# Kernel optimization log

Measured on AMD Instinct MI355X. Metric: run time of the kernel, lower is better.

The kernel has to match this reference:

```python
import jax, jax.numpy as jnp
import numpy as np

B, C, H, W = 8, 256, 64, 64
IC = C // 2  # inter_channel


def setup_inputs() -> dict:
    key = jax.random.key(0)
    k0, k1, k2, k3, k4 = jax.random.split(key, 5)
    s = 0.05
    return {
        "x": jax.random.normal(k0, (B, C, H, W), dtype=jnp.float32),
        "w_theta": jax.random.normal(k1, (IC, C), dtype=jnp.float32) * s,
        "w_phi": jax.random.normal(k2, (IC, C), dtype=jnp.float32) * s,
        "w_g": jax.random.normal(k3, (IC, C), dtype=jnp.float32) * s,
        "w_mask": jax.random.normal(k4, (C, IC), dtype=jnp.float32) * s,
    }


def reference(x, w_theta, w_phi, w_g, w_mask):
    b, c, h, w = x.shape
    ic = c // 2
    # 1x1 convs (bias=False) == channel-mixing einsums -> (b, ic, h, w)
    theta = jnp.einsum("oc,bchw->bohw", w_theta, x)
    phi = jnp.einsum("oc,bchw->bohw", w_phi, x)
    g = jnp.einsum("oc,bchw->bohw", w_g, x)
    # Faithful to original: .view(b, c, -1) on a (b, ic, h, w) tensor
    # => sequence length N = h*w/2, feature dim = c (full channels).
    n = ic * h * w // c  # = h*w/2
    x_theta = theta.reshape(b, c, n).transpose(0, 2, 1)  # (b, n, c)
    x_phi = phi.reshape(b, c, n)                          # (b, c, n)
    x_g = g.reshape(b, c, n).transpose(0, 2, 1)           # (b, n, c)
    attn = jnp.matmul(x_theta, x_phi)                     # (b, n, n)
    # Original uses nn.Softmax(dim=1): normalize over ROWS, not last axis.
    attn = jax.nn.softmax(attn, axis=1)
    out = jnp.matmul(attn, x_g)                           # (b, n, c)
    out = out.transpose(0, 2, 1).reshape(b, ic, h, w)     # (b, ic, h, w)
    mask = jnp.einsum("oc,bchw->bohw", w_mask, out)       # (b, c, h, w)
    return mask + x
```

## Files before the change

kernel.cpp:

```cpp
#include <hip/hip_runtime.h>

typedef __attribute__((ext_vector_type(8))) __bf16 bf16x8;
typedef __attribute__((ext_vector_type(4))) float f32x4;

#define LOG2E 1.4426950408889634f

#define OTA_OFF  0ul
#define TT_OFF   16777216ul
#define PT_OFF   25165824ul
#define G_OFF    33554432ul
#define W3_OFF   41943040ul
#define WM_OFF   42139648ul
#define ID_OFF   42205184ul
#define PART_OFF 42270720ul
#define WS_NEED  44367872ul

__device__ __forceinline__ void gload16(const __bf16* g, __bf16* l){
  __builtin_amdgcn_global_load_lds((const __attribute__((address_space(1))) void*)g,
                                   (__attribute__((address_space(3))) void*)l, 16, 0, 0);
}

__global__ __launch_bounds__(256) void k_weights(const float* wt, const float* wp,
                                                 const float* wg, const float* wm,
                                                 __bf16* W3, __bf16* Wm){
  int idx = blockIdx.x*256 + threadIdx.x;
  if (idx < 98304){
    float v = (idx < 32768) ? wt[idx] : (idx < 65536) ? wp[idx - 32768] : wg[idx - 65536];
    W3[idx] = (__bf16)v;
  } else if (idx < 131072){
    Wm[idx - 98304] = (__bf16)wm[idx - 98304];
  }
}

__global__ __launch_bounds__(512, 2) void k_conv3x(const float* x, const __bf16* W3,
                                                   __bf16* Tt, __bf16* Pt, __bf16* G){
  __shared__ __bf16 As[128*256];
  __shared__ __bf16 Bs[2][64*256];
  __shared__ float  tf[64*65];
  int bid = blockIdx.x;
  int b = bid & 7, m = bid >> 3, p0 = m*128;
  int tid = threadIdx.x, lane = tid & 63, w = tid >> 6;
  int lr = lane & 15, kq = lane >> 4;
  int pw = w & 1, ow4 = w >> 1;
  const float* xb = x + (size_t)b*256*4096 + p0;
  int sRow2 = lane >> 5, sSlot = lane & 31;
  #pragma unroll
  for (int u = 0; u < 4; ++u){
    int row = u*16 + w*2 + sRow2;
    gload16(W3 + (size_t)row*256 + ((sSlot ^ (row & 7))*8), &Bs[0][(u*16 + w*2)*256]);
  }
  #pragma unroll
  for (int st = 0; st < 8; ++st){
    int ct = st >> 1, pt = st & 1;
    int c0 = ct*64, ps = pt*64;
    #pragma unroll
    for (int u = 0; u < 2; ++u){
      int idx = u*512 + tid;
      int row = idx >> 4, col4 = (idx & 15)*4;
      f32x4 v = *(const f32x4*)(xb + (size_t)(c0 + row)*4096 + ps + col4);
      #pragma unroll
      for (int e = 0; e < 4; ++e) tf[row*65 + col4 + e] = v[e];
    }
    __syncthreads();
    {
      int pl = tid & 63, slot8 = tid >> 6;
      __bf16 pk[8];
      #pragma unroll
      for (int e = 0; e < 8; ++e) pk[e] = (__bf16)tf[(slot8*8 + e)*65 + pl];
      int row = ps + pl, slotIdx = ct*8 + slot8;
      *(uint4*)&As[row*256 + ((slotIdx ^ (row & 7))*8)] = *(const uint4*)pk;
    }
    __syncthreads();
  }
  bf16x8 aReg[4][8];
  #pragma unroll
  for (int fm = 0; fm < 4; ++fm){
    int ar = pw*64 + fm*16 + lr;
    #pragma unroll
    for (int sl = 0; sl < 8; ++sl){
      int slotA = (sl >> 1)*8 + (sl & 1)*4 + kq;
      aReg[fm][sl] = *(const bf16x8*)&As[ar*256 + ((slotA ^ (ar & 7))*8)];
    }
  }
  for (int ot = 0; ot < 6; ++ot){
    if (ot < 5){
      int buf = (ot + 1) & 1;
      #pragma unroll
      for (int u = 0; u < 4; ++u){
        int row = u*16 + w*2 + sRow2;
        gload16(W3 + (size_t)((ot+1)*64 + row)*256 + ((sSlot ^ (row & 7))*8),
                &Bs[buf][(u*16 + w*2)*256]);
      }
    }
    const __bf16* Bc = &Bs[ot & 1][0];
    f32x4 acc[4] = {};
    #pragma unroll
    for (int kc = 0; kc < 4; ++kc)
      #pragma unroll
      for (int ks = 0; ks < 2; ++ks){
        int slotB = kc*8 + ks*4 + kq;
        int br = ow4*16 + lr;
        bf16x8 bf = *(const bf16x8*)&Bc[br*256 + ((slotB ^ (br & 7))*8)];
        #pragma unroll
        for (int fm = 0; fm < 4; ++fm)
          acc[fm] = __builtin_amdgcn_mfma_f32_16x16x32_bf16(aReg[fm][kc*2+ks], bf, acc[fm], 0, 0, 0);
      }
    #pragma unroll
    for (int fm = 0; fm < 4; ++fm)
      #pragma unroll
      for (int r = 0; r < 4; ++r){
        int p = p0 + pw*64 + fm*16 + kq*4 + r;
        int o = ot*64 + ow4*16 + lr;
        __bf16 v = (__bf16)acc[fm][r];
        int i = p & 2047, ph = p >> 11;
        if (o < 128)      Tt[((size_t)b*2048 + i)*256 + 2*o + ph] = v;
        else if (o < 256) Pt[((size_t)b*2048 + i)*256 + 2*(o-128) + ph] = v;
        else              G [((size_t)b*256 + 2*(o-256) + ph)*2048 + i] = v;
      }
    __syncthreads();
  }
}

__global__ __launch_bounds__(512, 2) void k_sexp(const __bf16* Tt, const __bf16* Pt,
                                                 __bf16* S, float* PART, int js0){
  __shared__ __bf16 As[64*256];
  __shared__ __bf16 Bs[8][3][2048];
  int bid = blockIdx.x;
  int b = bid & 7, m = bid >> 3, m0 = m*64;
  int tid = threadIdx.x, lane = tid & 63, w = tid >> 6;
  int lr = lane & 15, kq = lane >> 4;
  const __bf16* Ab = Tt + ((size_t)b*2048 + m0)*256;
  const __bf16* Pb = Pt + ((size_t)b*2048 + js0)*256;
  __bf16* Sb = S + ((size_t)b*2048 + m0)*1024;
  {
    int aRow = lane >> 5, aSlot = lane & 31;
    #pragma unroll
    for (int u = 0; u < 4; ++u){
      int row = w*8 + u*2 + aRow;
      gload16(Ab + (size_t)row*256 + ((aSlot ^ (row & 7))*8), &As[w*2048 + u*512]);
    }
  }
  int bRow = lane >> 3, bSlot = lane & 7;
  #pragma unroll
  for (int s0 = 0; s0 < 2; ++s0){
    int j0 = (w + (s0 >> 2)*8)*32, kc = s0 & 3;
    #pragma unroll
    for (int u = 0; u < 4; ++u){
      int row = j0 + u*8 + bRow;
      gload16(Pb + (size_t)row*256 + kc*64 + ((bSlot ^ (row & 7))*8), &Bs[w][s0][u*512]);
    }
  }
  __syncthreads();
  bf16x8 aReg[4][8];
  #pragma unroll
  for (int fm = 0; fm < 4; ++fm){
    int ar = fm*16 + lr;
    #pragma unroll
    for (int sl = 0; sl < 8; ++sl){
      int slotA = (sl >> 1)*8 + (sl & 1)*4 + kq;
      aReg[fm][sl] = *(const bf16x8*)&As[ar*256 + ((slotA ^ (ar & 7))*8)];
    }
  }
  for (int q = 0; q < 4; ++q){
    int j0 = (w + q*8)*32;
    f32x4 acc[4][2] = {};
    #pragma unroll
    for (int kc = 0; kc < 4; ++kc){
      int s = q*4 + kc;
      if (s == 15) asm volatile("s_waitcnt vmcnt(0)" ::: "memory");
      else         asm volatile("s_waitcnt vmcnt(4)" ::: "memory");
      if (s + 2 < 16){
        int s2 = s + 2, q2 = s2 >> 2, kc2 = s2 & 3, rb = s2 % 3;
        int j02 = (w + q2*8)*32;
        #pragma unroll
        for (int u = 0; u < 4; ++u){
          int row = j02 + u*8 + bRow;
          gload16(Pb + (size_t)row*256 + kc2*64 + ((bSlot ^ (row & 7))*8), &Bs[w][rb][u*512]);
        }
      }
      const __bf16* Bc = &Bs[w][s % 3][0];
      #pragma unroll
      for (int ks = 0; ks < 2; ++ks){
        int slotB = ks*4 + kq;
        bf16x8 bf[2];
        #pragma unroll
        for (int fn = 0; fn < 2; ++fn){
          int br = fn*16 + lr;
          bf[fn] = *(const bf16x8*)&Bc[br*64 + ((slotB ^ (br & 7))*8)];
        }
        #pragma unroll
        for (int fm = 0; fm < 4; ++fm)
          #pragma unroll
          for (int fn = 0; fn < 2; ++fn)
            acc[fm][fn] = __builtin_amdgcn_mfma_f32_16x16x32_bf16(aReg[fm][kc*2+ks], bf[fn], acc[fm][fn], 0, 0, 0);
      }
    }
    #pragma unroll
    for (int fn = 0; fn < 2; ++fn){
      float v = 0.f;
      #pragma unroll
      for (int fm = 0; fm < 4; ++fm){
        #pragma unroll
        for (int r = 0; r < 4; ++r){
          float e = exp2f(acc[fm][fn][r] * LOG2E);
          v += e;
          Sb[(size_t)(fm*16 + kq*4 + r)*1024 + j0 + fn*16 + lr] = (__bf16)e;
        }
      }
      v += __shfl_xor(v, 16);
      v += __shfl_xor(v, 32);
      if (kq == 0)
        PART[((size_t)b*32 + m)*1024 + j0 + fn*16 + lr] = v;
    }
  }
}

__global__ __launch_bounds__(256) void k_invd(const float* PART, float* invD, int js0){
  int bid = blockIdx.x;
  int b = bid & 7, seg = bid >> 3;
  int jl = seg*256 + threadIdx.x;
  float s = 0.f;
  #pragma unroll
  for (int it = 0; it < 32; ++it) s += PART[((size_t)b*32 + it)*1024 + jl];
  invD[(size_t)b*2048 + js0 + jl] = 1.0f / s;
}

__global__ __launch_bounds__(256) void k_gscale(__bf16* G, const float* invD, int js0){
  int bid = blockIdx.x;
  int b = bid >> 8, c = bid & 255;
  int jl = threadIdx.x * 4;
  __bf16* gp = G + ((size_t)b*256 + c)*2048 + js0 + jl;
  const float* dp = invD + (size_t)b*2048 + js0 + jl;
  f32x4 d = *(const f32x4*)dp;
  __bf16 gv[4];
  *(uint2*)gv = *(const uint2*)gp;
  #pragma unroll
  for (int e = 0; e < 4; ++e) gv[e] = (__bf16)((float)gv[e] * d[e]);
  *(uint2*)gp = *(const uint2*)gv;
}

__global__ __launch_bounds__(256) void k_pv(const __bf16* S, const __bf16* G,
                                            float* OTacc, int js0, int first){
  __shared__ __bf16 sA[3][128*64];
  __shared__ __bf16 sB[3][64*64];
  int bid = blockIdx.x;
  int b = bid & 7, r2 = bid >> 3;
  int n = r2 & 3, m = r2 >> 2;
  int m0 = m*128, n0 = n*64;
  int tid = threadIdx.x, lane = tid & 63, w = tid >> 6;
  int lr = lane & 15, kq = lane >> 4;
  int wm = w >> 1, wn = w & 1;
  const __bf16* Ab = S + ((size_t)b*2048 + m0)*1024;
  const __bf16* Bb = G + ((size_t)b*256 + n0)*2048 + js0;
  int bRow = lane >> 3, bSlot = lane & 7;
  f32x4 acc[4][2] = {};
  #pragma unroll
  for (int t0 = 0; t0 < 2; ++t0){
    #pragma unroll
    for (int u = 0; u < 4; ++u){
      int row = u*32 + w*8 + bRow;
      gload16(Ab + (size_t)row*1024 + t0*64 + ((bSlot ^ (row & 7))*8),
              &sA[t0][u*2048 + w*512]);
    }
    #pragma unroll
    for (int u = 0; u < 2; ++u){
      int row = u*32 + w*8 + bRow;
      gload16(Bb + (size_t)row*2048 + t0*64 + ((bSlot ^ (row & 7))*8),
              &sB[t0][u*2048 + w*512]);
    }
  }
  for (int t = 0; t < 16; ++t){
    if (t == 15) asm volatile("s_waitcnt vmcnt(0)" ::: "memory");
    else         asm volatile("s_waitcnt vmcnt(6)" ::: "memory");
    __builtin_amdgcn_s_barrier();
    if (t + 2 < 16){
      int t2 = t + 2, bf2 = t2 % 3, k0 = t2*64;
      #pragma unroll
      for (int u = 0; u < 4; ++u){
        int row = u*32 + w*8 + bRow;
        gload16(Ab + (size_t)row*1024 + k0 + ((bSlot ^ (row & 7))*8),
                &sA[bf2][u*2048 + w*512]);
      }
      #pragma unroll
      for (int u = 0; u < 2; ++u){
        int row = u*32 + w*8 + bRow;
        gload16(Bb + (size_t)row*2048 + k0 + ((bSlot ^ (row & 7))*8),
                &sB[bf2][u*2048 + w*512]);
      }
    }
    const __bf16* Ac = &sA[t % 3][0];
    const __bf16* Bc = &sB[t % 3][0];
    #pragma unroll
    for (int ks = 0; ks < 2; ++ks){
      int slot = ks*4 + kq;
      bf16x8 af[4], bf[2];
      #pragma unroll
      for (int fm = 0; fm < 4; ++fm){
        int ar = wm*64 + fm*16 + lr;
        af[fm] = *(const bf16x8*)&Ac[ar*64 + ((slot ^ (ar & 7))*8)];
      }
      #pragma unroll
      for (int fn = 0; fn < 2; ++fn){
        int br = wn*32 + fn*16 + lr;
        bf[fn] = *(const bf16x8*)&Bc[br*64 + ((slot ^ (br & 7))*8)];
      }
      #pragma unroll
      for (int fm = 0; fm < 4; ++fm)
        #pragma unroll
        for (int fn = 0; fn < 2; ++fn)
          acc[fm][fn] = __builtin_amdgcn_mfma_f32_16x16x32_bf16(af[fm], bf[fn], acc[fm][fn], 0, 0, 0);
    }
  }
  float* Ob = OTacc + (size_t)b*4096*128;
  if (first){
    #pragma unroll
    for (int fm = 0; fm < 4; ++fm)
      #pragma unroll
      for (int fn = 0; fn < 2; ++fn)
        #pragma unroll
        for (int r = 0; r < 4; ++r){
          int i = m0 + wm*64 + fm*16 + kq*4 + r;
          int c = n0 + wn*32 + fn*16 + lr;
          Ob[(size_t)(((c & 1) << 11) + i)*128 + (c >> 1)] = acc[fm][fn][r];
        }
  } else {
    #pragma unroll
    for (int fm = 0; fm < 4; ++fm)
      #pragma unroll
      for (int fn = 0; fn < 2; ++fn)
        #pragma unroll
        for (int r = 0; r < 4; ++r){
          int i = m0 + wm*64 + fm*16 + kq*4 + r;
          int c = n0 + wn*32 + fn*16 + lr;
          size_t idx = (size_t)(((c & 1) << 11) + i)*128 + (c >> 1);
          Ob[idx] += acc[fm][fn][r];
        }
  }
}

__global__ __launch_bounds__(256) void k_mask(const float* OTacc, const __bf16* Wm,
                                              const float* x, float* out){
  __shared__ __bf16 As[128*72];
  __shared__ __bf16 Bs[64*72];
  int b = blockIdx.z, p0 = blockIdx.x*128, o0 = blockIdx.y*64;
  int tid = threadIdx.x, lane = tid & 63, wave = tid >> 6;
  int wm = wave >> 1, wn = wave & 1;
  f32x4 acc[4][2] = {};
  const float* Ab = OTacc + ((size_t)b*4096 + p0)*128;
  const __bf16* Bb = Wm + (size_t)o0*128;
  for (int kc = 0; kc < 2; ++kc){
    int k0 = kc*64;
    #pragma unroll
    for (int it = 0; it < 8; ++it){
      int idx = it*256 + tid;
      int row = idx >> 4, c4 = (idx & 15)*4;
      f32x4 vv = *(const f32x4*)(Ab + (size_t)row*128 + k0 + c4);
      __bf16 tmp[4];
      #pragma unroll
      for (int e = 0; e < 4; ++e) tmp[e] = (__bf16)vv[e];
      *(uint2*)&As[row*72 + c4] = *(const uint2*)tmp;
    }
    #pragma unroll
    for (int itc = 0; itc < 2; ++itc){
      int s = tid + itc*256, row = s >> 3, sk = s & 7;
      *(uint4*)&Bs[row*72 + sk*8] = *(const uint4*)(Bb + (size_t)row*128 + k0 + sk*8);
    }
    __syncthreads();
    #pragma unroll
    for (int ks = 0; ks < 2; ++ks){
      int koff = ks*32 + (lane>>4)*8;
      bf16x8 af[4], bfr[2];
      #pragma unroll
      for (int fm = 0; fm < 4; ++fm)
        af[fm] = *(const bf16x8*)&As[(wm*64 + fm*16 + (lane&15))*72 + koff];
      #pragma unroll
      for (int fn = 0; fn < 2; ++fn)
        bfr[fn] = *(const bf16x8*)&Bs[(wn*32 + fn*16 + (lane&15))*72 + koff];
      #pragma unroll
      for (int fm = 0; fm < 4; ++fm)
        #pragma unroll
        for (int fn = 0; fn < 2; ++fn)
          acc[fm][fn] = __builtin_amdgcn_mfma_f32_16x16x32_bf16(af[fm], bfr[fn], acc[fm][fn], 0, 0, 0);
    }
    __syncthreads();
  }
  #pragma unroll
  for (int fm = 0; fm < 4; ++fm)
    #pragma unroll
    for (int fn = 0; fn < 2; ++fn){
      int pb = p0 + wm*64 + fm*16 + (lane>>4)*4;
      int o = o0 + wn*32 + fn*16 + (lane&15);
      size_t idx = ((size_t)b*256 + o)*4096 + pb;
      f32x4 xv = *(const f32x4*)(x + idx);
      f32x4 ov = acc[fm][fn] + xv;
      *(f32x4*)(out + idx) = ov;
    }
}

extern "C" void kernel_launch(void* const* d_in, const int* in_sizes, int n_in,
                              void* d_out, int out_size, void* d_ws, size_t ws_size,
                              hipStream_t stream){
  if (ws_size < WS_NEED) return;
  const float* x  = (const float*)d_in[0];
  const float* wt = (const float*)d_in[1];
  const float* wp = (const float*)d_in[2];
  const float* wg = (const float*)d_in[3];
  const float* wm = (const float*)d_in[4];
  char* ws = (char*)d_ws;
  float* OTacc = (float*)(ws + OTA_OFF);
  __bf16* Tt   = (__bf16*)(ws + TT_OFF);
  __bf16* Pt   = (__bf16*)(ws + PT_OFF);
  __bf16* G    = (__bf16*)(ws + G_OFF);
  __bf16* W3   = (__bf16*)(ws + W3_OFF);
  __bf16* Wm   = (__bf16*)(ws + WM_OFF);
  float* invD  = (float*)(ws + ID_OFF);
  float* PART  = (float*)(ws + PART_OFF);
  __bf16* S    = (__bf16*)d_out;
  float* out   = (float*)d_out;

  k_weights<<<512, 256, 0, stream>>>(wt, wp, wg, wm, W3, Wm);
  k_conv3x<<<256, 512, 0, stream>>>(x, W3, Tt, Pt, G);
  for (int s = 0; s < 2; ++s){
    int js0 = s * 1024;
    k_sexp<<<256, 512, 0, stream>>>(Tt, Pt, S, PART, js0);
    k_invd<<<32, 256, 0, stream>>>(PART, invD, js0);
    k_gscale<<<2048, 256, 0, stream>>>(G, invD, js0);
    k_pv<<<512, 256, 0, stream>>>(S, G, OTacc, js0, s == 0 ? 1 : 0);
  }
  k_mask<<<dim3(32, 4, 8), 256, 0, stream>>>(OTacc, Wm, x, out);
}
```

Measured before the change: 134.7 us.

## Load A fragments directly to registers and deepen B prefetch to four stages

```diff
diff --git a/kernel.cpp b/kernel.cpp
--- a/kernel.cpp
+++ b/kernel.cpp
@@ -123,62 +123,51 @@
 
 __global__ __launch_bounds__(512, 2) void k_sexp(const __bf16* Tt, const __bf16* Pt,
                                                  __bf16* S, float* PART, int js0){
-  __shared__ __bf16 As[64*256];
-  __shared__ __bf16 Bs[8][3][2048];
+  __shared__ __bf16 Bs[8][4][2048];
   int bid = blockIdx.x;
   int b = bid & 7, m = bid >> 3, m0 = m*64;
   int tid = threadIdx.x, lane = tid & 63, w = tid >> 6;
   int lr = lane & 15, kq = lane >> 4;
-  const __bf16* Ab = Tt + ((size_t)b*2048 + m0)*256;
+  const __bf16* Tb = Tt + ((size_t)b*2048 + m0)*256;
   const __bf16* Pb = Pt + ((size_t)b*2048 + js0)*256;
   __bf16* Sb = S + ((size_t)b*2048 + m0)*1024;
-  {
-    int aRow = lane >> 5, aSlot = lane & 31;
-    #pragma unroll
-    for (int u = 0; u < 4; ++u){
-      int row = w*8 + u*2 + aRow;
-      gload16(Ab + (size_t)row*256 + ((aSlot ^ (row & 7))*8), &As[w*2048 + u*512]);
-    }
-  }
+  bf16x8 aReg[4][8];
+  #pragma unroll
+  for (int fm = 0; fm < 4; ++fm)
+    #pragma unroll
+    for (int sl = 0; sl < 8; ++sl)
+      aReg[fm][sl] = *(const bf16x8*)(Tb + (size_t)(fm*16 + lr)*256
+                                      + (sl >> 1)*64 + (sl & 1)*32 + kq*8);
   int bRow = lane >> 3, bSlot = lane & 7;
   #pragma unroll
-  for (int s0 = 0; s0 < 2; ++s0){
-    int j0 = (w + (s0 >> 2)*8)*32, kc = s0 & 3;
+  for (int s0 = 0; s0 < 3; ++s0){
+    int j0 = w*32, kc = s0;
     #pragma unroll
     for (int u = 0; u < 4; ++u){
       int row = j0 + u*8 + bRow;
       gload16(Pb + (size_t)row*256 + kc*64 + ((bSlot ^ (row & 7))*8), &Bs[w][s0][u*512]);
     }
   }
-  __syncthreads();
-  bf16x8 aReg[4][8];
-  #pragma unroll
-  for (int fm = 0; fm < 4; ++fm){
-    int ar = fm*16 + lr;
-    #pragma unroll
-    for (int sl = 0; sl < 8; ++sl){
-      int slotA = (sl >> 1)*8 + (sl & 1)*4 + kq;
-      aReg[fm][sl] = *(const bf16x8*)&As[ar*256 + ((slotA ^ (ar & 7))*8)];
-    }
-  }
   for (int q = 0; q < 4; ++q){
     int j0 = (w + q*8)*32;
     f32x4 acc[4][2] = {};
     #pragma unroll
     for (int kc = 0; kc < 4; ++kc){
       int s = q*4 + kc;
-      if (s == 15) asm volatile("s_waitcnt vmcnt(0)" ::: "memory");
-      else         asm volatile("s_waitcnt vmcnt(4)" ::: "memory");
-      if (s + 2 < 16){
-        int s2 = s + 2, q2 = s2 >> 2, kc2 = s2 & 3, rb = s2 % 3;
+      if (s < 14)       asm volatile("s_waitcnt vmcnt(8)" ::: "memory");
+      else if (s == 14) asm volatile("s_waitcnt vmcnt(4)" ::: "memory");
+      else              asm volatile("s_waitcnt vmcnt(0)" ::: "memory");
+      if (s + 3 < 16){
+        int s2 = s + 3, q2 = s2 >> 2, kc2 = s2 & 3;
         int j02 = (w + q2*8)*32;
         #pragma unroll
         for (int u = 0; u < 4; ++u){
           int row = j02 + u*8 + bRow;
-          gload16(Pb + (size_t)row*256 + kc2*64 + ((bSlot ^ (row & 7))*8), &Bs[w][rb][u*512]);
+          gload16(Pb + (size_t)row*256 + kc2*64 + ((bSlot ^ (row & 7))*8),
+                  &Bs[w][s2 & 3][u*512]);
         }
       }
-      const __bf16* Bc = &Bs[w][s % 3][0];
+      const __bf16* Bc = &Bs[w][s & 3][0];
       #pragma unroll
       for (int ks = 0; ks < 2; ++ks){
         int slotB = ks*4 + kq;
```

After: 142.5 us. 5.8% more time.

## Halve k_sexp row tile and double-buffer P to raise occupancy

Applied to the files above, without the earlier changes.

```diff
diff --git a/kernel.cpp b/kernel.cpp
--- a/kernel.cpp
+++ b/kernel.cpp
@@ -121,12 +121,12 @@
   }
 }
 
-__global__ __launch_bounds__(512, 2) void k_sexp(const __bf16* Tt, const __bf16* Pt,
+__global__ __launch_bounds__(512, 4) void k_sexp(const __bf16* Tt, const __bf16* Pt,
                                                  __bf16* S, float* PART, int js0){
-  __shared__ __bf16 As[64*256];
-  __shared__ __bf16 Bs[8][3][2048];
+  __shared__ __bf16 As[32*256];
+  __shared__ __bf16 Bs[8][2][2048];
   int bid = blockIdx.x;
-  int b = bid & 7, m = bid >> 3, m0 = m*64;
+  int b = bid & 7, m = bid >> 3, m0 = m*32;
   int tid = threadIdx.x, lane = tid & 63, w = tid >> 6;
   int lr = lane & 15, kq = lane >> 4;
   const __bf16* Ab = Tt + ((size_t)b*2048 + m0)*256;
@@ -135,71 +135,68 @@
   {
     int aRow = lane >> 5, aSlot = lane & 31;
     #pragma unroll
-    for (int u = 0; u < 4; ++u){
-      int row = w*8 + u*2 + aRow;
-      gload16(Ab + (size_t)row*256 + ((aSlot ^ (row & 7))*8), &As[w*2048 + u*512]);
+    for (int u = 0; u < 2; ++u){
+      int row = w*4 + u*2 + aRow;
+      gload16(Ab + (size_t)row*256 + ((aSlot ^ (row & 7))*8), &As[w*1024 + u*512]);
     }
   }
   int bRow = lane >> 3, bSlot = lane & 7;
-  #pragma unroll
-  for (int s0 = 0; s0 < 2; ++s0){
-    int j0 = (w + (s0 >> 2)*8)*32, kc = s0 & 3;
+  {
+    int j0 = w*32;
     #pragma unroll
     for (int u = 0; u < 4; ++u){
       int row = j0 + u*8 + bRow;
-      gload16(Pb + (size_t)row*256 + kc*64 + ((bSlot ^ (row & 7))*8), &Bs[w][s0][u*512]);
+      gload16(Pb + (size_t)row*256 + ((bSlot ^ (row & 7))*8), &Bs[w][0][u*512]);
     }
   }
   __syncthreads();
-  bf16x8 aReg[4][8];
-  #pragma unroll
-  for (int fm = 0; fm < 4; ++fm){
-    int ar = fm*16 + lr;
-    #pragma unroll
-    for (int sl = 0; sl < 8; ++sl){
-      int slotA = (sl >> 1)*8 + (sl & 1)*4 + kq;
-      aReg[fm][sl] = *(const bf16x8*)&As[ar*256 + ((slotA ^ (ar & 7))*8)];
-    }
-  }
   for (int q = 0; q < 4; ++q){
     int j0 = (w + q*8)*32;
-    f32x4 acc[4][2] = {};
+    f32x4 acc[2][2] = {};
     #pragma unroll
     for (int kc = 0; kc < 4; ++kc){
       int s = q*4 + kc;
-      if (s == 15) asm volatile("s_waitcnt vmcnt(0)" ::: "memory");
-      else         asm volatile("s_waitcnt vmcnt(4)" ::: "memory");
-      if (s + 2 < 16){
-        int s2 = s + 2, q2 = s2 >> 2, kc2 = s2 & 3, rb = s2 % 3;
+      if (s + 1 < 16){
+        int s2 = s + 1, q2 = s2 >> 2, kc2 = s2 & 3;
         int j02 = (w + q2*8)*32;
         #pragma unroll
         for (int u = 0; u < 4; ++u){
           int row = j02 + u*8 + bRow;
-          gload16(Pb + (size_t)row*256 + kc2*64 + ((bSlot ^ (row & 7))*8), &Bs[w][rb][u*512]);
-        }
-      }
-      const __bf16* Bc = &Bs[w][s % 3][0];
+          gload16(Pb + (size_t)row*256 + kc2*64 + ((bSlot ^ (row & 7))*8),
+                  &Bs[w][s2 & 1][u*512]);
+        }
+        asm volatile("s_waitcnt vmcnt(4)" ::: "memory");
+      } else {
+        asm volatile("s_waitcnt vmcnt(0)" ::: "memory");
+      }
+      const __bf16* Bc = &Bs[w][s & 1][0];
       #pragma unroll
       for (int ks = 0; ks < 2; ++ks){
+        int slotA = kc*8 + ks*4 + kq;
         int slotB = ks*4 + kq;
-        bf16x8 bf[2];
+        bf16x8 af[2], bf[2];
+        #pragma unroll
+        for (int fm = 0; fm < 2; ++fm){
+          int ar = fm*16 + lr;
+          af[fm] = *(const bf16x8*)&As[ar*256 + ((slotA ^ (ar & 7))*8)];
+        }
         #pragma unroll
         for (int fn = 0; fn < 2; ++fn){
           int br = fn*16 + lr;
           bf[fn] = *(const bf16x8*)&Bc[br*64 + ((slotB ^ (br & 7))*8)];
         }
         #pragma unroll
-        for (int fm = 0; fm < 4; ++fm)
+        for (int fm = 0; fm < 2; ++fm)
           #pragma unroll
           for (int fn = 0; fn < 2; ++fn)
-            acc[fm][fn] = __builtin_amdgcn_mfma_f32_16x16x32_bf16(aReg[fm][kc*2+ks], bf[fn], acc[fm][fn], 0, 0, 0);
+            acc[fm][fn] = __builtin_amdgcn_mfma_f32_16x16x32_bf16(af[fm], bf[fn], acc[fm][fn], 0, 0, 0);
       }
     }
     #pragma unroll
     for (int fn = 0; fn < 2; ++fn){
       float v = 0.f;
       #pragma unroll
-      for (int fm = 0; fm < 4; ++fm){
+      for (int fm = 0; fm < 2; ++fm){
         #pragma unroll
         for (int r = 0; r < 4; ++r){
           float e = exp2f(acc[fm][fn][r] * LOG2E);
@@ -210,7 +207,7 @@
       v += __shfl_xor(v, 16);
       v += __shfl_xor(v, 32);
       if (kq == 0)
-        PART[((size_t)b*32 + m)*1024 + j0 + fn*16 + lr] = v;
+        PART[((size_t)b*64 + m)*1024 + j0 + fn*16 + lr] = v;
     }
   }
 }
@@ -221,7 +218,7 @@
   int jl = seg*256 + threadIdx.x;
   float s = 0.f;
   #pragma unroll
-  for (int it = 0; it < 32; ++it) s += PART[((size_t)b*32 + it)*1024 + jl];
+  for (int it = 0; it < 64; ++it) s += PART[((size_t)b*64 + it)*1024 + jl];
   invD[(size_t)b*2048 + js0 + jl] = 1.0f / s;
 }
 
@@ -422,7 +419,7 @@
   k_conv3x<<<256, 512, 0, stream>>>(x, W3, Tt, Pt, G);
   for (int s = 0; s < 2; ++s){
     int js0 = s * 1024;
-    k_sexp<<<256, 512, 0, stream>>>(Tt, Pt, S, PART, js0);
+    k_sexp<<<512, 512, 0, stream>>>(Tt, Pt, S, PART, js0);
     k_invd<<<32, 256, 0, stream>>>(PART, invD, js0);
     k_gscale<<<2048, 256, 0, stream>>>(G, invD, js0);
     k_pv<<<512, 256, 0, stream>>>(S, G, OTacc, js0, s == 0 ? 1 : 0);
```

New measurement: 136.3 us. No clear change (+1.2%).
